# Performance work log

Measured on AMD Instinct MI355X. Metric: run time of the kernel, lower is better.

The kernel has to match this reference:

```python
import jax, jax.numpy as jnp
import numpy as np

B, C, H, W = 16, 256, 64, 64
NH = 4                      # num_heads
HD = C // NH                # head_dim = 64
G = 32                      # GroupNorm groups
EPS = 1e-5


def setup_inputs() -> dict:
    key = jax.random.key(0)
    ks = jax.random.split(key, 7)
    x = jax.random.normal(ks[0], (B, C, H, W), dtype=jnp.float32)
    gn_w = jnp.ones((C,), dtype=jnp.float32)
    gn_b = jnp.zeros((C,), dtype=jnp.float32)
    qkv_w = jax.random.normal(ks[1], (3 * C, C), dtype=jnp.float32) * 0.02
    qkv_b = jnp.zeros((3 * C,), dtype=jnp.float32)
    out_w = jax.random.normal(ks[2], (C, C), dtype=jnp.float32) * 0.02
    out_b = jnp.zeros((C,), dtype=jnp.float32)
    return {"x": x, "gn_w": gn_w, "gn_b": gn_b, "qkv_w": qkv_w,
            "qkv_b": qkv_b, "out_w": out_w, "out_b": out_b}


def _group_norm(x, w, b):
    # x: (B, C, H, W); normalize over each of G groups of channels (+ spatial)
    Bx, Cx, Hx, Wx = x.shape
    xr = x.reshape(Bx, G, -1)
    mean = xr.mean(axis=-1, keepdims=True)
    var = xr.var(axis=-1, keepdims=True)
    h = ((xr - mean) * jax.lax.rsqrt(var + EPS)).reshape(Bx, Cx, Hx, Wx)
    return h * w[None, :, None, None] + b[None, :, None, None]


def reference(x, gn_w, gn_b, qkv_w, qkv_b, out_w, out_b):
    Bx, Cx, Hx, Wx = x.shape
    N = Hx * Wx
    h = _group_norm(x, gn_w, gn_b)
    # 1x1 conv == channel matmul
    qkv = jnp.einsum('oc,bchw->bohw', qkv_w, h) + qkv_b[None, :, None, None]
    q, k, v = jnp.split(qkv, 3, axis=1)
    # b (h d) y x -> b h d n
    q = q.reshape(Bx, NH, HD, N)
    k = k.reshape(Bx, NH, HD, N)
    v = v.reshape(Bx, NH, HD, N)
    q = jax.nn.softmax(q, axis=-1)   # over spatial positions n
    k = jax.nn.softmax(k, axis=-2)   # over head_dim d
    # context = k @ v^T : (b,h,d,d)
    context = jnp.einsum('bhdn,bhen->bhde', k, v)
    # out = context^T @ q : (b,h,d,n)
    out = jnp.einsum('bhde,bhdn->bhen', context, q)
    out = out.reshape(Bx, Cx, Hx, Wx)
    out = jnp.einsum('oc,bchw->bohw', out_w, out) + out_b[None, :, None, None]
    return x + out
```

## Files before the change

kernel.cpp:

```cpp
#include <hip/hip_runtime.h>


typedef __bf16 bf16x8 __attribute__((ext_vector_type(8)));
typedef __bf16 bf16x4 __attribute__((ext_vector_type(4)));
typedef __bf16 bf16x2 __attribute__((ext_vector_type(2)));
typedef float  f32x4  __attribute__((ext_vector_type(4)));

__device__ __forceinline__ float wave_red_sum(float v) {
#pragma unroll
    for (int off = 32; off > 0; off >>= 1) v += __shfl_xor(v, off, 64);
    return v;
}
__device__ __forceinline__ float wave_red_max(float v) {
#pragma unroll
    for (int off = 32; off > 0; off >>= 1) v = fmaxf(v, __shfl_xor(v, off, 64));
    return v;
}

__global__ __launch_bounds__(256)
void gn_stats_kernel(const float* __restrict__ x, const float* __restrict__ gw,
                     const float* __restrict__ gb, const float* __restrict__ qw,
                     float2* __restrict__ scsh, __bf16* __restrict__ wb)
{
    const int blk = blockIdx.x;
    const int b = blk >> 5, g = blk & 31;
    const int tid = threadIdx.x;
    const int lane = tid & 63, wid = tid >> 6;
    const size_t xbase = ((size_t)(b * 256 + g * 8)) * 4096;

    {
        const int ci = (blk * 256 + tid) * 2;
        if (ci < 196608) {
            const float2 f = *(const float2*)(qw + ci);
            bf16x2 t; t[0] = (__bf16)f.x; t[1] = (__bf16)f.y;
            *(bf16x2*)(wb + ci) = t;
        }
    }

    float s1 = 0.f, s2 = 0.f;
#pragma unroll
    for (int it = 0; it < 32; it++) {
        const int idx = (it * 256 + tid) * 4;
        const float4 v4 = *(const float4*)(x + xbase + idx);
        s1 += v4.x + v4.y + v4.z + v4.w;
        s2 += v4.x * v4.x + v4.y * v4.y + v4.z * v4.z + v4.w * v4.w;
    }
    __shared__ float red[8];
    float s1w = wave_red_sum(s1);
    float s2w = wave_red_sum(s2);
    if (lane == 0) { red[wid] = s1w; red[4 + wid] = s2w; }
    __syncthreads();
    const float mean = (red[0] + red[1] + red[2] + red[3]) * (1.0f / 32768.0f);
    const float ms   = (red[4] + red[5] + red[6] + red[7]) * (1.0f / 32768.0f);
    const float inv  = rsqrtf(fmaxf(ms - mean * mean, 0.f) + 1e-5f);

    if (tid < 8) {
        const int c = g * 8 + tid;
        const float sc = gw[c] * inv;
        const float sh = gb[c] - mean * sc;
        scsh[b * 256 + c] = make_float2(sc, sh);
    }
}

__global__ __launch_bounds__(256)
void gemm1_kernel(const __bf16* __restrict__ wbf,
                  const float* __restrict__ x,
                  const float* __restrict__ bias,
                  const float2* __restrict__ scsh,
                  __bf16* __restrict__ qkv)
{
    __shared__ __align__(16) __bf16 lds_bt[64 * 264];
    __shared__ __align__(16) char  lds_a[256 * 64];
    __shared__ float2 lscsh[256];

    const int tid  = threadIdx.x;
    const int lane = tid & 63;
    const int wid  = tid >> 6;
    const int quad = lane >> 4;
    const int tcol = lane & 15;
    const int wm   = wid * 64;
    const int n0   = blockIdx.x * 64;
    const int b    = n0 >> 12;
    const int nn   = n0 & 4095;

    lscsh[tid] = scsh[b * 256 + tid];
    __syncthreads();

    const int sn = tid & 63;
    const int cq = tid >> 6;
    const float* xs = x + (size_t)b * 1048576 + nn + sn;
#pragma unroll
    for (int iter = 0; iter < 4; iter++) {
        const int cbase = cq * 64 + iter * 16;
        bf16x8 o0, o1;
#pragma unroll
        for (int j = 0; j < 16; j++) {
            const int c = cbase + j;
            const float2 ss = lscsh[c];
            const float f = xs[(size_t)c * 4096];
            const __bf16 v = (__bf16)(f * ss.x + ss.y);
            if (j < 8) o0[j] = v; else o1[j - 8] = v;
        }
        __bf16* dst = &lds_bt[sn * 264 + cbase];
        *(bf16x8*)dst       = o0;
        *(bf16x8*)(dst + 8) = o1;
    }

    const int r_   = tid >> 1;
    const int ah   = tid & 1;
    const int h16  = ah * 16;
    const int aswz = (r_ >> 1) & 3;
    const int ch0  = (((ah * 2)     + aswz) & 3) * 16;
    const int ch1  = (((ah * 2 + 1) + aswz) & 3) * 16;
    const __bf16* abase = wbf + (size_t)r_ * 256 + h16;

    bf16x8 a0 = *(const bf16x8*)(abase);
    bf16x8 a1 = *(const bf16x8*)(abase + 8);
    bf16x8 a2 = *(const bf16x8*)(abase + 32768);
    bf16x8 a3 = *(const bf16x8*)(abase + 32768 + 8);

    for (int mt = 0; mt < 3; mt++) {
        f32x4 acc[4][4];
#pragma unroll
        for (int i = 0; i < 4; i++)
#pragma unroll
            for (int j = 0; j < 4; j++) acc[i][j] = {0.f, 0.f, 0.f, 0.f};

        for (int kt = 0; kt < 256; kt += 32) {
            __syncthreads();
            *(bf16x8*)&lds_a[r_ * 64         + ch0] = a0;
            *(bf16x8*)&lds_a[r_ * 64         + ch1] = a1;
            *(bf16x8*)&lds_a[(r_ + 128) * 64 + ch0] = a2;
            *(bf16x8*)&lds_a[(r_ + 128) * 64 + ch1] = a3;
            __syncthreads();

            const int last = (kt == 224);
            const int nkt  = last ? 0 : kt + 32;
            const int nmt  = last ? mt + 1 : mt;
            if (nmt < 3) {
                const __bf16* ap = abase + (size_t)nmt * 65536 + nkt;
                a0 = *(const bf16x8*)(ap);
                a1 = *(const bf16x8*)(ap + 8);
                a2 = *(const bf16x8*)(ap + 32768);
                a3 = *(const bf16x8*)(ap + 32768 + 8);
            }

            bf16x8 af[4];
#pragma unroll
            for (int mi = 0; mi < 4; mi++) {
                const int m = wm + mi * 16 + tcol;
                af[mi] = *(const bf16x8*)&lds_a[m * 64
                         + ((quad + ((m >> 1) & 3)) & 3) * 16];
            }
            bf16x8 bfr[4];
#pragma unroll
            for (int ni = 0; ni < 4; ni++)
                bfr[ni] = *(const bf16x8*)&lds_bt[(ni * 16 + tcol) * 264
                                                 + kt + quad * 8];
#pragma unroll
            for (int mi = 0; mi < 4; mi++)
#pragma unroll
                for (int ni = 0; ni < 4; ni++)
                    acc[mi][ni] = __builtin_amdgcn_mfma_f32_16x16x32_bf16(
                        af[mi], bfr[ni], acc[mi][ni], 0, 0, 0);
        }

#pragma unroll
        for (int mi = 0; mi < 4; mi++) {
#pragma unroll
            for (int r = 0; r < 4; r++) {
                const int grow = mt * 256 + wm + mi * 16 + quad * 4 + r;
                const float bv = bias[grow];
#pragma unroll
                for (int ni = 0; ni < 4; ni++) {
                    const int gcol = n0 + ni * 16 + tcol;
                    qkv[(size_t)grow * 65536 + gcol] = (__bf16)(acc[mi][ni][r] + bv);
                }
            }
        }
    }
}

__global__ __launch_bounds__(256)
void qstats_kernel(const __bf16* __restrict__ qkv, float2* __restrict__ qst)
{
    const int o = blockIdx.x >> 4;
    const int b = blockIdx.x & 15;
    const int tid = threadIdx.x;
    const int lane = tid & 63, wid = tid >> 6;
    const size_t base = (size_t)o * 65536 + (size_t)b * 4096;

    float v[16];
    float m = -INFINITY;
#pragma unroll
    for (int s = 0; s < 16; s++) {
        v[s] = (float)qkv[base + s * 256 + tid];
        m = fmaxf(m, v[s]);
    }
    __shared__ float red[4];
    float wmx = wave_red_max(m);
    if (lane == 0) red[wid] = wmx;
    __syncthreads();
    m = fmaxf(fmaxf(red[0], red[1]), fmaxf(red[2], red[3]));
    __syncthreads();
    float sum = 0.f;
#pragma unroll
    for (int s = 0; s < 16; s++) sum += __expf(v[s] - m);
    float wsm = wave_red_sum(sum);
    if (lane == 0) red[wid] = wsm;
    __syncthreads();
    if (tid == 0)
        qst[o * 16 + b] = make_float2(m, 1.0f / (red[0] + red[1] + red[2] + red[3]));
}

__global__ __launch_bounds__(256)
void ctx_mfma_kernel(const __bf16* __restrict__ qkv, float* __restrict__ ctx)
{
    const int bh = blockIdx.x >> 3, kc = blockIdx.x & 7;
    const int b = bh >> 2, hh = bh & 3;
    __shared__ __align__(16) __bf16 lk[64 * 72], lv[64 * 72];
    __shared__ float smax[4][64], ssum[4][64];
    const int tid = threadIdx.x;
    const int lane = tid & 63, wid = tid >> 6;
    const int quad = lane >> 4, tcol = lane & 15;
    const int eh = (wid & 1) * 32, dh = (wid >> 1) * 32;
    const int col = tid & 63, dq = tid >> 6;
    const int sd = tid >> 2, snn = (tid & 3) * 16;

    f32x4 acc[2][2];
#pragma unroll
    for (int i = 0; i < 2; i++)
#pragma unroll
        for (int j = 0; j < 2; j++) acc[i][j] = {0.f, 0.f, 0.f, 0.f};

    const size_t kbase = (size_t)(256 + hh * 64) * 65536 + (size_t)b * 4096 + kc * 512;
    const size_t vbase = (size_t)(512 + hh * 64) * 65536 + (size_t)b * 4096 + kc * 512;

    for (int nc = 0; nc < 512; nc += 64) {
        __syncthreads();
        {
            const __bf16* ks = qkv + kbase + (size_t)sd * 65536 + nc + snn;
            *(bf16x8*)&lk[sd * 72 + snn]     = *(const bf16x8*)ks;
            *(bf16x8*)&lk[sd * 72 + snn + 8] = *(const bf16x8*)(ks + 8);
            const __bf16* vs = qkv + vbase + (size_t)sd * 65536 + nc + snn;
            *(bf16x8*)&lv[sd * 72 + snn]     = *(const bf16x8*)vs;
            *(bf16x8*)&lv[sd * 72 + snn + 8] = *(const bf16x8*)(vs + 8);
        }
        __syncthreads();

        float kvv[16];
        float pm = -INFINITY;
#pragma unroll
        for (int i = 0; i < 16; i++) {
            kvv[i] = (float)lk[(dq * 16 + i) * 72 + col];
            pm = fmaxf(pm, kvv[i]);
        }
        smax[dq][col] = pm;
        __syncthreads();
        const float m = fmaxf(fmaxf(smax[0][col], smax[1][col]),
                              fmaxf(smax[2][col], smax[3][col]));
        float ps = 0.f;
#pragma unroll
        for (int i = 0; i < 16; i++) { kvv[i] = __expf(kvv[i] - m); ps += kvv[i]; }
        ssum[dq][col] = ps;
        __syncthreads();
        const float inv = 1.0f / (ssum[0][col] + ssum[1][col] + ssum[2][col] + ssum[3][col]);
#pragma unroll
        for (int i = 0; i < 16; i++)
            lk[(dq * 16 + i) * 72 + col] = (__bf16)(kvv[i] * inv);
        __syncthreads();

#pragma unroll
        for (int k2 = 0; k2 < 64; k2 += 32) {
            bf16x8 af[2], bfr[2];
#pragma unroll
            for (int mi = 0; mi < 2; mi++)
                af[mi] = *(const bf16x8*)&lv[(eh + mi * 16 + tcol) * 72 + k2 + quad * 8];
#pragma unroll
            for (int ni = 0; ni < 2; ni++)
                bfr[ni] = *(const bf16x8*)&lk[(dh + ni * 16 + tcol) * 72 + k2 + quad * 8];
#pragma unroll
            for (int mi = 0; mi < 2; mi++)
#pragma unroll
                for (int ni = 0; ni < 2; ni++)
                    acc[mi][ni] = __builtin_amdgcn_mfma_f32_16x16x32_bf16(
                        af[mi], bfr[ni], acc[mi][ni], 0, 0, 0);
        }
    }
    float* cb = ctx + (size_t)bh * 4096;
#pragma unroll
    for (int mi = 0; mi < 2; mi++)
#pragma unroll
        for (int ni = 0; ni < 2; ni++)
#pragma unroll
            for (int r = 0; r < 4; r++) {
                const int e = eh + mi * 16 + quad * 4 + r;
                const int d = dh + ni * 16 + tcol;
                atomicAdd(&cb[e * 64 + d], acc[mi][ni][r]);
            }
}

__global__ __launch_bounds__(256)
void w2_kernel(const float* __restrict__ ctx, const float* __restrict__ out_w,
               __bf16* __restrict__ w2)
{
    const int bh = blockIdx.x;
    const int b = bh >> 2, hh = bh & 3;
    const int tid = threadIdx.x;

    __shared__ __align__(16) float lctx[4096];
    const float* csrc = ctx + (size_t)bh * 4096;
#pragma unroll
    for (int i = 0; i < 4; i++)
        ((float4*)lctx)[tid + i * 256] = ((const float4*)csrc)[tid + i * 256];
    __syncthreads();

    float acc[64];
#pragma unroll
    for (int d = 0; d < 64; d++) acc[d] = 0.f;

    const float* wrow = out_w + (size_t)tid * 256 + hh * 64;
    for (int e = 0; e < 64; e++) {
        const float w = wrow[e];
#pragma unroll
        for (int d4 = 0; d4 < 64; d4 += 4) {
            const float4 c4 = *(const float4*)&lctx[e * 64 + d4];
            acc[d4 + 0] += w * c4.x;
            acc[d4 + 1] += w * c4.y;
            acc[d4 + 2] += w * c4.z;
            acc[d4 + 3] += w * c4.w;
        }
    }
    __bf16* dst = w2 + (size_t)b * 65536 + (size_t)tid * 256 + hh * 64;
#pragma unroll
    for (int d4 = 0; d4 < 64; d4 += 4) {
        bf16x4 t;
        t[0] = (__bf16)acc[d4 + 0]; t[1] = (__bf16)acc[d4 + 1];
        t[2] = (__bf16)acc[d4 + 2]; t[3] = (__bf16)acc[d4 + 3];
        *(bf16x4*)(dst + d4) = t;
    }
}

__global__ __launch_bounds__(256)
void gemm2_kernel(const __bf16* __restrict__ w2,
                  const __bf16* __restrict__ qkv,
                  const float2* __restrict__ qst,
                  const float* __restrict__ bias,
                  const float* __restrict__ xres,
                  float* __restrict__ out)
{
    __shared__ __align__(16) __bf16 lds_bt[64 * 264];
    __shared__ __align__(16) char  lds_a[256 * 64];
    __shared__ float2 lqst[256];

    const int tid  = threadIdx.x;
    const int lane = tid & 63;
    const int wid  = tid >> 6;
    const int quad = lane >> 4;
    const int tcol = lane & 15;
    const int wm   = wid * 64;
    const int n0   = blockIdx.x * 64;
    const int b    = n0 >> 12;

    lqst[tid] = qst[tid * 16 + b];
    __syncthreads();

    const int pr  = tid & 31;
    const int cg  = tid >> 5;
    const int sn0 = pr * 2;
    const __bf16* qs = qkv + n0 + sn0;
#pragma unroll
    for (int cc = 0; cc < 32; cc += 8) {
        bf16x8 oe, oo;
#pragma unroll
        for (int j = 0; j < 8; j++) {
            const int c = cg * 32 + cc + j;
            const float2 qq = lqst[c];
            const bf16x2 u = *(const bf16x2*)(qs + (size_t)c * 65536);
            oe[j] = (__bf16)(__expf((float)u[0] - qq.x) * qq.y);
            oo[j] = (__bf16)(__expf((float)u[1] - qq.x) * qq.y);
        }
        *(bf16x8*)&lds_bt[sn0 * 264 + cg * 32 + cc]       = oe;
        *(bf16x8*)&lds_bt[(sn0 + 1) * 264 + cg * 32 + cc] = oo;
    }

    const int r_   = tid >> 1;
    const int ah   = tid & 1;
    const int h16  = ah * 16;
    const int aswz = (r_ >> 1) & 3;
    const int ch0  = (((ah * 2)     + aswz) & 3) * 16;
    const int ch1  = (((ah * 2 + 1) + aswz) & 3) * 16;
    const __bf16* abase = w2 + (size_t)b * 65536 + (size_t)r_ * 256 + h16;

    bf16x8 a0 = *(const bf16x8*)(abase);
    bf16x8 a1 = *(const bf16x8*)(abase + 8);
    bf16x8 a2 = *(const bf16x8*)(abase + 32768);
    bf16x8 a3 = *(const bf16x8*)(abase + 32768 + 8);

    f32x4 acc[4][4];
#pragma unroll
    for (int i = 0; i < 4; i++)
#pragma unroll
        for (int j = 0; j < 4; j++) acc[i][j] = {0.f, 0.f, 0.f, 0.f};

    for (int kt = 0; kt < 256; kt += 32) {
        __syncthreads();
        *(bf16x8*)&lds_a[r_ * 64         + ch0] = a0;
        *(bf16x8*)&lds_a[r_ * 64         + ch1] = a1;
        *(bf16x8*)&lds_a[(r_ + 128) * 64 + ch0] = a2;
        *(bf16x8*)&lds_a[(r_ + 128) * 64 + ch1] = a3;
        __syncthreads();

        if (kt < 224) {
            const __bf16* ap = abase + kt + 32;
            a0 = *(const bf16x8*)(ap);
            a1 = *(const bf16x8*)(ap + 8);
            a2 = *(const bf16x8*)(ap + 32768);
            a3 = *(const bf16x8*)(ap + 32768 + 8);
        }

        bf16x8 af[4];
#pragma unroll
        for (int mi = 0; mi < 4; mi++) {
            const int m = wm + mi * 16 + tcol;
            af[mi] = *(const bf16x8*)&lds_a[m * 64
                     + ((quad + ((m >> 1) & 3)) & 3) * 16];
        }
        bf16x8 bfr[4];
#pragma unroll
        for (int ni = 0; ni < 4; ni++)
            bfr[ni] = *(const bf16x8*)&lds_bt[(ni * 16 + tcol) * 264
                                             + kt + quad * 8];
#pragma unroll
        for (int mi = 0; mi < 4; mi++)
#pragma unroll
            for (int ni = 0; ni < 4; ni++)
                acc[mi][ni] = __builtin_amdgcn_mfma_f32_16x16x32_bf16(
                    af[mi], bfr[ni], acc[mi][ni], 0, 0, 0);
    }

#pragma unroll
    for (int mi = 0; mi < 4; mi++) {
#pragma unroll
        for (int r = 0; r < 4; r++) {
            const int grow = wm + mi * 16 + quad * 4 + r;
            const float bv = bias[grow];
#pragma unroll
            for (int ni = 0; ni < 4; ni++) {
                const int n = (n0 & 4095) + ni * 16 + tcol;
                const size_t oidx = ((size_t)(b * 256 + grow)) * 4096 + n;
                out[oidx] = acc[mi][ni][r] + bv + xres[oidx];
            }
        }
    }
}

extern "C" void kernel_launch(void* const* d_in, const int* in_sizes, int n_in,
                              void* d_out, int out_size, void* d_ws, size_t ws_size,
                              hipStream_t stream)
{
    const float* x     = (const float*)d_in[0];
    const float* gn_w  = (const float*)d_in[1];
    const float* gn_b  = (const float*)d_in[2];
    const float* qkv_w = (const float*)d_in[3];
    const float* qkv_b = (const float*)d_in[4];
    const float* out_w = (const float*)d_in[5];
    const float* out_b = (const float*)d_in[6];
    float* out = (float*)d_out;

    char* ws = (char*)d_ws;
    __bf16* qkv  = (__bf16*)ws;
    float*  ctx  = (float*)(ws + (size_t)100663296);
    float2* scsh = (float2*)(ws + (size_t)101711872);
    float2* qst  = (float2*)(ws + (size_t)101744640);
    __bf16* wbf  = (__bf16*)(ws + (size_t)101777408);
    __bf16* w2   = qkv + (size_t)256 * 65536;

    hipMemsetAsync(ctx, 0, 262144 * sizeof(float), stream);
    gn_stats_kernel<<<512, 256, 0, stream>>>(x, gn_w, gn_b, qkv_w, scsh, wbf);
    gemm1_kernel<<<1024, 256, 0, stream>>>(wbf, x, qkv_b, scsh, qkv);
    qstats_kernel<<<4096, 256, 0, stream>>>(qkv, qst);
    ctx_mfma_kernel<<<512, 256, 0, stream>>>(qkv, ctx);
    w2_kernel<<<64, 256, 0, stream>>>(ctx, out_w, w2);
    gemm2_kernel<<<1024, 256, 0, stream>>>(w2, qkv, qst, out_b, x, out);
}
```

Measured before the change: 263.6 us.

## Stage GEMM epilogues through LDS for coalesced stores; precompute k softmax stats

Both GEMM epilogues now write their accumulators into swizzled LDS first and then emit wide vectorized row-contiguous global stores. The second GEMM also reads the residual with float4 loads, which replaces scattered per-element writes. The per-column k softmax max and sum move out of ctx_mfma_kernel into a new kstats_kernel that writes them to a scratch buffer in d_out. ctx_mfma_kernel then applies exp-normalization while loading, which removes three barriers and the LDS reduction rounds per chunk. The cost is an extra kernel launch, strided k reads in kstats, and extra syncs in the epilogues.

```diff
diff --git a/kernel.cpp b/kernel.cpp
--- a/kernel.cpp
+++ b/kernel.cpp
@@ -166,15 +166,34 @@
         }
 
 #pragma unroll
-        for (int mi = 0; mi < 4; mi++) {
-#pragma unroll
-            for (int r = 0; r < 4; r++) {
-                const int grow = mt * 256 + wm + mi * 16 + quad * 4 + r;
-                const float bv = bias[grow];
-#pragma unroll
-                for (int ni = 0; ni < 4; ni++) {
-                    const int gcol = n0 + ni * 16 + tcol;
-                    qkv[(size_t)grow * 65536 + gcol] = (__bf16)(acc[mi][ni][r] + bv);
+        for (int half = 0; half < 2; half++) {
+            __syncthreads();
+            if ((wm >> 7) == half) {
+                const int rbase = wm & 127;
+#pragma unroll
+                for (int mi = 0; mi < 4; mi++)
+#pragma unroll
+                    for (int r = 0; r < 4; r++) {
+                        const int row  = rbase + mi * 16 + quad * 4 + r;
+                        const int grow = mt * 256 + half * 128 + row;
+                        const float bv = bias[grow];
+#pragma unroll
+                        for (int ni = 0; ni < 4; ni++) {
+                            const int col  = ni * 16 + tcol;
+                            const int byo  = (row * 128 + col * 2) ^ ((row & 7) << 4);
+                            *(__bf16*)&lds_a[byo] = (__bf16)(acc[mi][ni][r] + bv);
+                        }
+                    }
+            }
+            __syncthreads();
+            {
+                const int row  = tid >> 1, seg = tid & 1;
+                const int grow = mt * 256 + half * 128 + row;
+                __bf16* dst = qkv + (size_t)grow * 65536 + n0 + seg * 32;
+#pragma unroll
+                for (int j = 0; j < 4; j++) {
+                    const int byo = (row * 128 + seg * 64 + j * 16) ^ ((row & 7) << 4);
+                    *(bf16x8*)(dst + j * 8) = *(const bf16x8*)&lds_a[byo];
                 }
             }
         }
@@ -214,17 +233,35 @@
 }
 
 __global__ __launch_bounds__(256)
-void ctx_mfma_kernel(const __bf16* __restrict__ qkv, float* __restrict__ ctx)
+void kstats_kernel(const __bf16* __restrict__ qkv, float2* __restrict__ kst)
+{
+    const int bh = blockIdx.x >> 4, chunk = blockIdx.x & 15;
+    const int b = bh >> 2, hh = bh & 3;
+    const int n = chunk * 256 + threadIdx.x;
+    const __bf16* kp = qkv + (size_t)(256 + hh * 64) * 65536 + (size_t)b * 4096 + n;
+
+    float m = -INFINITY;
+    for (int d = 0; d < 64; d++)
+        m = fmaxf(m, (float)kp[(size_t)d * 65536]);
+    float s = 0.f;
+    for (int d = 0; d < 64; d++)
+        s += __expf((float)kp[(size_t)d * 65536] - m);
+    kst[(size_t)bh * 4096 + n] = make_float2(m, 1.0f / s);
+}
+
+__global__ __launch_bounds__(256)
+void ctx_mfma_kernel(const __bf16* __restrict__ qkv,
+                     const float2* __restrict__ kst,
+                     float* __restrict__ ctx)
 {
     const int bh = blockIdx.x >> 3, kc = blockIdx.x & 7;
     const int b = bh >> 2, hh = bh & 3;
     __shared__ __align__(16) __bf16 lk[64 * 72], lv[64 * 72];
-    __shared__ float smax[4][64], ssum[4][64];
+    __shared__ float2 lsmv[2][64];
     const int tid = threadIdx.x;
     const int lane = tid & 63, wid = tid >> 6;
     const int quad = lane >> 4, tcol = lane & 15;
     const int eh = (wid & 1) * 32, dh = (wid >> 1) * 32;
-    const int col = tid & 63, dq = tid >> 6;
     const int sd = tid >> 2, snn = (tid & 3) * 16;
 
     f32x4 acc[2][2];
@@ -235,39 +272,33 @@
 
     const size_t kbase = (size_t)(256 + hh * 64) * 65536 + (size_t)b * 4096 + kc * 512;
     const size_t vbase = (size_t)(512 + hh * 64) * 65536 + (size_t)b * 4096 + kc * 512;
+    const float2* kstp = kst + (size_t)bh * 4096 + kc * 512;
+
+    if (tid < 64) lsmv[0][tid] = kstp[tid];
 
     for (int nc = 0; nc < 512; nc += 64) {
+        const int p = (nc >> 6) & 1;
         __syncthreads();
         {
             const __bf16* ks = qkv + kbase + (size_t)sd * 65536 + nc + snn;
-            *(bf16x8*)&lk[sd * 72 + snn]     = *(const bf16x8*)ks;
-            *(bf16x8*)&lk[sd * 72 + snn + 8] = *(const bf16x8*)(ks + 8);
+            const bf16x8 k0 = *(const bf16x8*)ks;
+            const bf16x8 k1 = *(const bf16x8*)(ks + 8);
+            bf16x8 o0, o1;
+#pragma unroll
+            for (int j = 0; j < 8; j++) {
+                const float2 s0 = lsmv[p][snn + j];
+                const float2 s1 = lsmv[p][snn + 8 + j];
+                o0[j] = (__bf16)(__expf((float)k0[j] - s0.x) * s0.y);
+                o1[j] = (__bf16)(__expf((float)k1[j] - s1.x) * s1.y);
+            }
+            *(bf16x8*)&lk[sd * 72 + snn]     = o0;
+            *(bf16x8*)&lk[sd * 72 + snn + 8] = o1;
             const __bf16* vs = qkv + vbase + (size_t)sd * 65536 + nc + snn;
             *(bf16x8*)&lv[sd * 72 + snn]     = *(const bf16x8*)vs;
             *(bf16x8*)&lv[sd * 72 + snn + 8] = *(const bf16x8*)(vs + 8);
         }
-        __syncthreads();
-
-        float kvv[16];
-        float pm = -INFINITY;
-#pragma unroll
-        for (int i = 0; i < 16; i++) {
-            kvv[i] = (float)lk[(dq * 16 + i) * 72 + col];
-            pm = fmaxf(pm, kvv[i]);
-        }
-        smax[dq][col] = pm;
-        __syncthreads();
-        const float m = fmaxf(fmaxf(smax[0][col], smax[1][col]),
-                              fmaxf(smax[2][col], smax[3][col]));
-        float ps = 0.f;
-#pragma unroll
-        for (int i = 0; i < 16; i++) { kvv[i] = __expf(kvv[i] - m); ps += kvv[i]; }
-        ssum[dq][col] = ps;
-        __syncthreads();
-        const float inv = 1.0f / (ssum[0][col] + ssum[1][col] + ssum[2][col] + ssum[3][col]);
-#pragma unroll
-        for (int i = 0; i < 16; i++)
-            lk[(dq * 16 + i) * 72 + col] = (__bf16)(kvv[i] * inv);
+        if (tid < 64 && nc + 64 < 512)
+            lsmv[p ^ 1][tid] = kstp[nc + 64 + tid];
         __syncthreads();
 
 #pragma unroll
@@ -440,16 +471,38 @@
     }
 
 #pragma unroll
-    for (int mi = 0; mi < 4; mi++) {
-#pragma unroll
-        for (int r = 0; r < 4; r++) {
-            const int grow = wm + mi * 16 + quad * 4 + r;
-            const float bv = bias[grow];
-#pragma unroll
-            for (int ni = 0; ni < 4; ni++) {
-                const int n = (n0 & 4095) + ni * 16 + tcol;
-                const size_t oidx = ((size_t)(b * 256 + grow)) * 4096 + n;
-                out[oidx] = acc[mi][ni][r] + bv + xres[oidx];
+    for (int rd = 0; rd < 4; rd++) {
+        __syncthreads();
+        if (wid == rd) {
+#pragma unroll
+            for (int mi = 0; mi < 4; mi++)
+#pragma unroll
+                for (int r = 0; r < 4; r++) {
+                    const int row = mi * 16 + quad * 4 + r;
+                    const float bv = bias[rd * 64 + row];
+#pragma unroll
+                    for (int ni = 0; ni < 4; ni++) {
+                        const int col = ni * 16 + tcol;
+                        const int byo = (row * 256 + col * 4) ^ ((row & 7) << 4);
+                        *(float*)&lds_a[byo] = acc[mi][ni][r] + bv;
+                    }
+                }
+        }
+        __syncthreads();
+        {
+            const int row = tid >> 2, q = tid & 3;
+            const int o = rd * 64 + row;
+            const size_t obase = ((size_t)(b * 256 + o)) * 4096
+                               + (n0 & 4095) + q * 16;
+#pragma unroll
+            for (int j = 0; j < 4; j++) {
+                const int byo = (row * 256 + q * 64 + j * 16) ^ ((row & 7) << 4);
+                const f32x4 v = *(const f32x4*)&lds_a[byo];
+                const float4 xv = *(const float4*)(xres + obase + j * 4);
+                float4 ov;
+                ov.x = v[0] + xv.x; ov.y = v[1] + xv.y;
+                ov.z = v[2] + xv.z; ov.w = v[3] + xv.w;
+                *(float4*)(out + obase + j * 4) = ov;
             }
         }
     }
@@ -475,12 +528,14 @@
     float2* qst  = (float2*)(ws + (size_t)101744640);
     __bf16* wbf  = (__bf16*)(ws + (size_t)101777408);
     __bf16* w2   = qkv + (size_t)256 * 65536;
+    float2* kst  = (float2*)d_out;
 
     hipMemsetAsync(ctx, 0, 262144 * sizeof(float), stream);
     gn_stats_kernel<<<512, 256, 0, stream>>>(x, gn_w, gn_b, qkv_w, scsh, wbf);
     gemm1_kernel<<<1024, 256, 0, stream>>>(wbf, x, qkv_b, scsh, qkv);
     qstats_kernel<<<4096, 256, 0, stream>>>(qkv, qst);
-    ctx_mfma_kernel<<<512, 256, 0, stream>>>(qkv, ctx);
+    kstats_kernel<<<1024, 256, 0, stream>>>(qkv, kst);
+    ctx_mfma_kernel<<<512, 256, 0, stream>>>(qkv, kst, ctx);
     w2_kernel<<<64, 256, 0, stream>>>(ctx, out_w, w2);
     gemm2_kernel<<<1024, 256, 0, stream>>>(w2, qkv, qst, out_b, x, out);
 }
```

New measurement: 346.7 us. +31.5%, slower.
